# Kernel optimization log

Measured on AMD Instinct MI355X. Metric: run time of the kernel, lower is better.

Reference implementation:

```python
import jax, jax.numpy as jnp
import numpy as np
import math

L, D, H, FF, V, S = 6, 512, 8, 2048, 32000, 1024
DH = D // H
EPS = 1e-5

def _ln(x, w, b):
    mu = jnp.mean(x, -1, keepdims=True)
    var = jnp.mean(jnp.square(x - mu), -1, keepdims=True)
    return (x - mu) * jax.lax.rsqrt(var + EPS) * w + b

def setup_inputs() -> dict:
    key = jax.random.key(0)
    ks = jax.random.split(key, 32)
    s = 0.02
    inp = {
        'x': jax.random.randint(ks[0], (4, S), 0, V, dtype=jnp.int32),
        'mask': jnp.ones((4, S), dtype=jnp.int32),
        'emb': jax.random.normal(ks[1], (V, D), jnp.float32) * s,
        'pos': jax.random.normal(ks[2], (S, D), jnp.float32) * s,
        'Wq': jax.random.normal(ks[3], (L, D, D), jnp.float32) * s,
        'bq': jnp.zeros((L, D), jnp.float32),
        'Wk': jax.random.normal(ks[4], (L, D, D), jnp.float32) * s,
        'bk': jnp.zeros((L, D), jnp.float32),
        'Wv': jax.random.normal(ks[5], (L, D, D), jnp.float32) * s,
        'bv': jnp.zeros((L, D), jnp.float32),
        'Wo': jax.random.normal(ks[6], (L, D, D), jnp.float32) * s,
        'bo': jnp.zeros((L, D), jnp.float32),
        'rel_bias': jax.random.normal(ks[7], (L, 2 * S - 1, H), jnp.float32) * s,
        'scale': jnp.full((L,), math.sqrt(DH), jnp.float32),
        'n1w': jnp.ones((L, D), jnp.float32), 'n1b': jnp.zeros((L, D), jnp.float32),
        'n2w': jnp.ones((L, D), jnp.float32), 'n2b': jnp.zeros((L, D), jnp.float32),
        'f1w': jax.random.normal(ks[8], (L, D, FF), jnp.float32) * s,
        'f1b': jnp.zeros((L, FF), jnp.float32),
        'f2w': jax.random.normal(ks[9], (L, FF, D), jnp.float32) * s,
        'f2b': jnp.zeros((L, D), jnp.float32),
        'fnw': jnp.ones((D,), jnp.float32), 'fnb': jnp.zeros((D,), jnp.float32),
        'fcw': jax.random.normal(ks[10], (D, V), jnp.float32) * s,
        'fcb': jnp.zeros((V,), jnp.float32),
    }
    return inp

def reference(x, mask, emb, pos, Wq, bq, Wk, bk, Wv, bv, Wo, bo, rel_bias, scale,
              n1w, n1b, n2w, n2b, f1w, f1b, f2w, f2b, fnw, fnb, fcw, fcb):
    B, seq = x.shape
    h = emb[x] * jnp.float32(math.sqrt(D)) + pos[None, :seq, :]
    # relative position index table: j - i + seq - 1, values in [0, 2*seq-2]
    r = jnp.arange(seq)
    rp = r[None, :] - r[:, None] + seq - 1  # (S, S)
    # pairwise valid mask (b,1,S,S)
    m2 = (mask[:, None, None, :] * mask[:, None, :, None]) != 0
    for l in range(L):
        q = (h @ Wq[l] + bq[l]).reshape(B, seq, H, DH)
        k = (h @ Wk[l] + bk[l]).reshape(B, seq, H, DH)
        v = (h @ Wv[l] + bv[l]).reshape(B, seq, H, DH)
        scores = jnp.einsum('bihd,bjhd->bhij', q, k) / scale[l]
        bias = rel_bias[l][rp]                      # (S,S,H)
        scores = scores + jnp.transpose(bias, (2, 0, 1))[None]
        scores = jnp.where(m2, scores, -jnp.inf)    # masked_fill(mask==0, -inf)
        attn = jnp.einsum('bhij,bjhd->bihd', scores, v).reshape(B, seq, D)
        attn = attn @ Wo[l] + bo[l]
        h = _ln(h + attn, n1w[l], n1b[l])
        ff = jax.nn.gelu(h @ f1w[l] + f1b[l], approximate=False) @ f2w[l] + f2b[l]
        h = _ln(h + ff, n2w[l], n2b[l])
    h = _ln(h, fnw, fnb)
    return h @ fcw + fcb
```

## Files before the change

kernel.cpp:

```cpp
#include <hip/hip_runtime.h>
#include <cmath>

#define S_LEN  1024
#define DMODEL 512
#define NHEAD  8
#define DHEAD  64
#define FFDIM  2048
#define VOCAB  32000
#define NLAYER 6
#define BATCHN 4
#define ROWS   (BATCHN * S_LEN)

typedef float    f32x4 __attribute__((ext_vector_type(4)));
typedef _Float16 f16x4 __attribute__((ext_vector_type(4)));
typedef _Float16 f16x8 __attribute__((ext_vector_type(8)));

__device__ __forceinline__ void glds16(const _Float16* g, _Float16* l) {
    __builtin_amdgcn_global_load_lds(
        (const __attribute__((address_space(1))) void*)g,
        (__attribute__((address_space(3))) void*)l, 16, 0, 0);
}

template<int N> __device__ __forceinline__ void waitvm() {
    if constexpr (N == 0)      asm volatile("s_waitcnt vmcnt(0)" ::: "memory");
    else if constexpr (N == 3) asm volatile("s_waitcnt vmcnt(3)" ::: "memory");
    else if constexpr (N == 4) asm volatile("s_waitcnt vmcnt(4)" ::: "memory");
    else if constexpr (N == 6) asm volatile("s_waitcnt vmcnt(6)" ::: "memory");
}

template<int WM, int WN, int MT, int NT, int EPI, int OUT16, int SWZ8>
__global__ __launch_bounds__(WM * WN * 64)
void pgemm_k(const _Float16* __restrict__ A, long lda,
             const _Float16* __restrict__ Bt, long ldb,
             void* __restrict__ Cg, long ldc, int K,
             const float* __restrict__ bias)
{
    constexpr int T   = WM * WN * 64;
    constexpr int BMt = WM * MT * 16;
    constexpr int BNt = WN * NT * 16;
    constexpr int SR  = T / 4;
    constexpr int RA  = BMt / SR;
    constexpr int RB  = BNt / SR;
    constexpr int L   = RA + RB;
    constexpr int ASZ = BMt * 32, BSZ = BNt * 32;

    __shared__ _Float16 As[3 * ASZ];
    __shared__ _Float16 Bs[3 * BSZ];

    int bx = blockIdx.x, by = blockIdx.y;
    if (SWZ8) {
        int nb  = gridDim.x * gridDim.y;
        int id  = by * gridDim.x + bx;
        int id2 = (id & 7) * (nb >> 3) + (id >> 3);
        bx = id2 % gridDim.x;
        by = id2 / gridDim.x;
    }
    const int m0 = bx * BMt, n0 = by * BNt;

    const int t = threadIdx.x, w = t >> 6, lane = t & 63;
    const int sub = t >> 2, ch = t & 3;
    const int wm = w / WN, wn = w % WN;
    const int wrow = wm * MT * 16, wcol = wn * NT * 16;
    const int lr = lane & 15, hk = lane >> 4;

    f32x4 acc[MT][NT];
#pragma unroll
    for (int i = 0; i < MT; i++)
#pragma unroll
        for (int j = 0; j < NT; j++) acc[i][j] = f32x4{0.f, 0.f, 0.f, 0.f};

    const int nst = K >> 5;

    auto stage = [&](int tt) {
        const int kt = tt << 5;
        _Float16* Ad = &As[(tt % 3) * ASZ];
        _Float16* Bd = &Bs[(tt % 3) * BSZ];
#pragma unroll
        for (int i = 0; i < RA; i++) {
            int lrow = i * SR + sub;
            glds16(A + (long)(m0 + lrow) * lda + kt + ((ch ^ ((lrow >> 1) & 3)) << 3),
                   Ad + (i * SR + w * 16) * 32);
        }
#pragma unroll
        for (int i = 0; i < RB; i++) {
            int lrow = i * SR + sub;
            glds16(Bt + (long)(n0 + lrow) * ldb + kt + ((ch ^ ((lrow >> 1) & 3)) << 3),
                   Bd + (i * SR + w * 16) * 32);
        }
    };

    stage(0);
    stage(1);

    for (int tt = 0; tt < nst; ++tt) {
        if (tt < nst - 1) waitvm<L>(); else waitvm<0>();
        asm volatile("s_barrier" ::: "memory");
        if (tt + 2 < nst) stage(tt + 2);

        const _Float16* Ar = &As[(tt % 3) * ASZ];
        const _Float16* Br = &Bs[(tt % 3) * BSZ];
        f16x8 af[MT], bf[NT];
#pragma unroll
        for (int mi = 0; mi < MT; mi++) {
            int r = wrow + mi * 16 + lr;
            af[mi] = *(const f16x8*)&Ar[r * 32 + ((hk ^ ((r >> 1) & 3)) << 3)];
        }
#pragma unroll
        for (int ni = 0; ni < NT; ni++) {
            int r = wcol + ni * 16 + lr;
            bf[ni] = *(const f16x8*)&Br[r * 32 + ((hk ^ ((r >> 1) & 3)) << 3)];
        }
#pragma unroll
        for (int mi = 0; mi < MT; mi++)
#pragma unroll
            for (int ni = 0; ni < NT; ni++)
                acc[mi][ni] = __builtin_amdgcn_mfma_f32_16x16x32_f16(af[mi], bf[ni], acc[mi][ni], 0, 0, 0);
    }

    const int crow = hk * 4, ccol = lr;
#pragma unroll
    for (int mi = 0; mi < MT; mi++)
#pragma unroll
        for (int ni = 0; ni < NT; ni++)
#pragma unroll
            for (int q = 0; q < 4; q++) {
                int gm = m0 + wrow + mi * 16 + crow + q;
                int gn = n0 + wcol + ni * 16 + ccol;
                float v = acc[mi][ni][q];
                if (bias) v += bias[gn];
                if (EPI == 2) v = 0.5f * v * (1.0f + erff(v * 0.70710678118654752f));
                long ci = (long)gm * ldc + gn;
                if (OUT16) ((_Float16*)Cg)[ci] = (_Float16)v;
                else       ((float*)Cg)[ci] = v;
            }
}

__global__ __launch_bounds__(256)
void ktv_k(const _Float16* __restrict__ kt, const _Float16* __restrict__ vt,
           _Float16* __restrict__ M, const float* __restrict__ scale_p)
{
    const int z = blockIdx.x;
    const int wave = threadIdx.x >> 6, lane = threadIdx.x & 63;
    const int lr = lane & 15, lk = (lane >> 4) * 8;
    const long base = (long)z * DHEAD * S_LEN;

    f32x4 acc[4];
#pragma unroll
    for (int i = 0; i < 4; i++) acc[i] = f32x4{0.f, 0.f, 0.f, 0.f};

    for (int j = 0; j < S_LEN; j += 32) {
        f16x8 a = *(const f16x8*)&vt[base + (long)(wave * 16 + lr) * S_LEN + j + lk];
#pragma unroll
        for (int ni = 0; ni < 4; ni++) {
            f16x8 b = *(const f16x8*)&kt[base + (long)(ni * 16 + lr) * S_LEN + j + lk];
            acc[ni] = __builtin_amdgcn_mfma_f32_16x16x32_f16(a, b, acc[ni], 0, 0, 0);
        }
    }

    const float inv = 1.0f / scale_p[0];
    const int crow = (lane >> 4) * 4, ccol = lane & 15;
#pragma unroll
    for (int ni = 0; ni < 4; ni++)
#pragma unroll
        for (int q = 0; q < 4; q++) {
            int gm = wave * 16 + crow + q;
            int gn = ni * 16 + ccol;
            M[(long)z * 4096 + (long)gm * 64 + gn] = (_Float16)(acc[ni][q] * inv);
        }
}

__global__ __launch_bounds__(256)
void toep_k(const _Float16* __restrict__ dv,
            const _Float16* __restrict__ vt,
            const _Float16* __restrict__ q,
            const _Float16* __restrict__ M,
            _Float16* __restrict__ ao)
{
    __shared__ _Float16 Qs[64 * 64];
    __shared__ _Float16 Ms[64 * 64];
    __shared__ _Float16 Vs[2][64 * 64];
    __shared__ _Float16 dseg[1088];

    const int t = threadIdx.x, w = t >> 6, lane = t & 63;
    const int z = blockIdx.z, zb = z >> 3, zh = z & 7;
    const int m0 = blockIdx.x * 64;
    const int lr = lane & 15, hk = lane >> 4;
    const int rsw = lr & 7;
    const int swz = ((lane & 7) ^ (lane >> 3)) * 8;
    const int wrow = w * 16;

    const _Float16* qa = q  + (long)(zb * S_LEN + m0 + w * 16 + (lane >> 3)) * 1536 + zh * 64 + swz;
    const _Float16* ma = M  + (long)z * 4096 + (long)(w * 16 + (lane >> 3)) * 64 + swz;
    const _Float16* va = vt + (long)z * (DHEAD * S_LEN) + (long)(w * 16 + (lane >> 3)) * S_LEN + swz;

#pragma unroll
    for (int i = 0; i < 2; i++) glds16(qa + (long)i * 8 * 1536, &Qs[(w * 16 + i * 8) * 64]);
#pragma unroll
    for (int i = 0; i < 2; i++) glds16(ma + i * 8 * 64, &Ms[(w * 16 + i * 8) * 64]);
#pragma unroll
    for (int i = 0; i < 2; i++) glds16(va + (long)i * 8 * S_LEN, &Vs[0][(w * 16 + i * 8) * 64]);
    {
        const _Float16* dp = dv + zh * 2048 + (960 - m0);
        for (int i = t; i < 1088; i += 256) dseg[i] = dp[i];
    }
    __syncthreads();

    f32x4 acc[4];
#pragma unroll
    for (int i = 0; i < 4; i++) acc[i] = f32x4{0.f, 0.f, 0.f, 0.f};

#pragma unroll
    for (int kc = 0; kc < 64; kc += 32) {
        const int coff = ((((kc >> 3) + hk) ^ rsw) << 3);
        f16x8 aq = *(const f16x8*)&Qs[(wrow + lr) * 64 + coff];
#pragma unroll
        for (int ni = 0; ni < 4; ni++) {
            f16x8 bm = *(const f16x8*)&Ms[(ni * 16 + lr) * 64 + coff];
            acc[ni] = __builtin_amdgcn_mfma_f32_16x16x32_f16(aq, bm, acc[ni], 0, 0, 0);
        }
    }

    int cur = 0;
    for (int kt = 0; kt < S_LEN; kt += 64) {
        if (kt + 64 < S_LEN) {
#pragma unroll
            for (int i = 0; i < 2; i++)
                glds16(va + (long)i * 8 * S_LEN + kt + 64, &Vs[cur ^ 1][(w * 16 + i * 8) * 64]);
        }
#pragma unroll
        for (int kc = 0; kc < 64; kc += 32) {
            const int coff = ((((kc >> 3) + hk) ^ rsw) << 3);
            f16x8 at_;
            const int xb = kt + kc + hk * 8 + 63 - wrow - lr;
#pragma unroll
            for (int u = 0; u < 8; u++) at_[u] = dseg[xb + u];
#pragma unroll
            for (int ni = 0; ni < 4; ni++) {
                f16x8 bv_ = *(const f16x8*)&Vs[cur][(ni * 16 + lr) * 64 + coff];
                acc[ni] = __builtin_amdgcn_mfma_f32_16x16x32_f16(at_, bv_, acc[ni], 0, 0, 0);
            }
        }
        __syncthreads();
        cur ^= 1;
    }

    const int crow = (lane >> 4) * 4, ccol = lane & 15;
    const long cbase = (long)zb * (S_LEN * DMODEL) + zh * DHEAD;
#pragma unroll
    for (int ni = 0; ni < 4; ni++)
#pragma unroll
        for (int qq = 0; qq < 4; qq++) {
            int gm = m0 + wrow + crow + qq;
            int gn = ni * 16 + ccol;
            ao[cbase + (long)gm * DMODEL + gn] = (_Float16)acc[ni][qq];
        }
}

__global__ void embed_k(const int* __restrict__ x, const float* __restrict__ emb,
                        const float* __restrict__ pos, float* __restrict__ h,
                        _Float16* __restrict__ h16)
{
    int row = blockIdx.x;
    int s   = row & (S_LEN - 1);
    int tok = x[row];
    int c   = threadIdx.x * 4;
    f32x4 e = *(const f32x4*)(emb + (long)tok * DMODEL + c);
    f32x4 p = *(const f32x4*)(pos + (long)s * DMODEL + c);
    f32x4 o = e * 22.62741699796952f + p;
    *(f32x4*)(h + (long)row * DMODEL + c) = o;
    f16x4 o16;
#pragma unroll
    for (int j = 0; j < 4; j++) o16[j] = (_Float16)o[j];
    *(f16x4*)(h16 + (long)row * DMODEL + c) = o16;
}

__global__ void ln_k(const float* __restrict__ x, const float* __restrict__ add,
                     const float* __restrict__ w, const float* __restrict__ bb,
                     float* __restrict__ out, _Float16* __restrict__ out16)
{
    int row  = blockIdx.x;
    int lane = threadIdx.x;
    const float* xp = x + (long)row * DMODEL + lane * 8;
    f32x4 a = *(const f32x4*)xp;
    f32x4 b4 = *(const f32x4*)(xp + 4);
    if (add) {
        const float* ap = add + (long)row * DMODEL + lane * 8;
        a  += *(const f32x4*)ap;
        b4 += *(const f32x4*)(ap + 4);
    }
    float v[8] = {a[0],a[1],a[2],a[3],b4[0],b4[1],b4[2],b4[3]};
    float s = 0.f;
#pragma unroll
    for (int i = 0; i < 8; i++) s += v[i];
#pragma unroll
    for (int off = 32; off; off >>= 1) s += __shfl_xor(s, off);
    float mu = s * (1.0f / 512.0f);
    float d2 = 0.f;
#pragma unroll
    for (int i = 0; i < 8; i++) { v[i] -= mu; d2 += v[i] * v[i]; }
#pragma unroll
    for (int off = 32; off; off >>= 1) d2 += __shfl_xor(d2, off);
    float r = rsqrtf(d2 * (1.0f / 512.0f) + 1e-5f);
    const float* wp = w  + lane * 8;
    const float* bp = bb + lane * 8;
    float o[8];
#pragma unroll
    for (int i = 0; i < 8; i++) o[i] = v[i] * r * wp[i] + bp[i];
    float* op = out + (long)row * DMODEL + lane * 8;
    *(f32x4*)op       = f32x4{o[0], o[1], o[2], o[3]};
    *(f32x4*)(op + 4) = f32x4{o[4], o[5], o[6], o[7]};
    f16x8 o16;
#pragma unroll
    for (int i = 0; i < 8; i++) o16[i] = (_Float16)o[i];
    *(f16x8*)(out16 + (long)row * DMODEL + lane * 8) = o16;
}

__global__ void wcvt_k(const float* __restrict__ in, _Float16* __restrict__ out,
                       int R, int C, long inZ, long outZ)
{
    __shared__ float tile[32][33];
    int z = blockIdx.z;
    int c0 = blockIdx.x * 32, r0 = blockIdx.y * 32;
    int tx = threadIdx.x, ty = threadIdx.y;
#pragma unroll
    for (int i = 0; i < 4; i++)
        tile[ty + i * 8][tx] = in[(long)z * inZ + (long)(r0 + ty + i * 8) * C + c0 + tx];
    __syncthreads();
#pragma unroll
    for (int i = 0; i < 4; i++)
        out[(long)z * outZ + (long)(c0 + ty + i * 8) * R + r0 + tx] = (_Float16)tile[tx][ty + i * 8];
}

__global__ void tv16_k(const _Float16* __restrict__ qkv,
                       _Float16* __restrict__ kt, _Float16* __restrict__ vt)
{
    __shared__ _Float16 tile[32][33];
    int z = blockIdx.z;
    const _Float16* v = qkv + ((z < 32) ? 512 : 1024);
    _Float16* dst = (z < 32) ? kt : vt;
    int zz = z & 31;
    int b = zz >> 3, hh = zz & 7;
    int j0 = blockIdx.x * 32, d0 = blockIdx.y * 32;
    long ibase = (long)b * S_LEN * 1536 + hh * DHEAD;
    long obase = (long)zz * (DHEAD * S_LEN);
    int tx = threadIdx.x, ty = threadIdx.y;
#pragma unroll
    for (int i = 0; i < 4; i++)
        tile[ty + i * 8][tx] = v[ibase + (long)(j0 + ty + i * 8) * 1536 + d0 + tx];
    __syncthreads();
#pragma unroll
    for (int i = 0; i < 4; i++)
        dst[obase + (long)(d0 + ty + i * 8) * S_LEN + j0 + tx] = tile[tx][ty + i * 8];
}

__global__ void bcat_k(const float* __restrict__ bq, const float* __restrict__ bk,
                       const float* __restrict__ bv, float* __restrict__ o)
{
    int l = blockIdx.x, t = threadIdx.x;
    o[l * 1536 + t]        = bq[l * 512 + t];
    o[l * 1536 + 512 + t]  = bk[l * 512 + t];
    o[l * 1536 + 1024 + t] = bv[l * 512 + t];
}

__global__ void dvec_k(const float* __restrict__ rel, _Float16* __restrict__ dv)
{
    int lh = blockIdx.x;
    int l = lh >> 3, hh = lh & 7;
    for (int t = threadIdx.x; t < 2048; t += 256)
        dv[(long)lh * 2048 + t] = (t < 2047) ? (_Float16)rel[(long)l * 2047 * 8 + (long)t * 8 + hh]
                                             : (_Float16)0.0f;
}

extern "C" void kernel_launch(void* const* d_in, const int* in_sizes, int n_in,
                              void* d_out, int out_size, void* d_ws, size_t ws_size,
                              hipStream_t stream)
{
    (void)in_sizes; (void)n_in; (void)out_size; (void)ws_size;

    const int*   x    = (const int*)d_in[0];
    const float* emb  = (const float*)d_in[2];
    const float* pos  = (const float*)d_in[3];
    const float* Wq   = (const float*)d_in[4];
    const float* bq   = (const float*)d_in[5];
    const float* Wk   = (const float*)d_in[6];
    const float* bk   = (const float*)d_in[7];
    const float* Wv   = (const float*)d_in[8];
    const float* bv   = (const float*)d_in[9];
    const float* Wo   = (const float*)d_in[10];
    const float* bo   = (const float*)d_in[11];
    const float* rel  = (const float*)d_in[12];
    const float* scal = (const float*)d_in[13];
    const float* n1w  = (const float*)d_in[14];
    const float* n1b  = (const float*)d_in[15];
    const float* n2w  = (const float*)d_in[16];
    const float* n2b  = (const float*)d_in[17];
    const float* f1w  = (const float*)d_in[18];
    const float* f1b  = (const float*)d_in[19];
    const float* f2w  = (const float*)d_in[20];
    const float* f2b  = (const float*)d_in[21];
    const float* fnw  = (const float*)d_in[22];
    const float* fnb  = (const float*)d_in[23];
    const float* fcw  = (const float*)d_in[24];
    const float* fcb  = (const float*)d_in[25];

    char* ws = (char*)d_ws;
    size_t off = 0;
    auto alloc = [&](size_t bytes) { char* p = ws + off; off += (bytes + 255) & ~(size_t)255; return p; };
    float*    h      = (float*)alloc((size_t)ROWS * DMODEL * 4);
    float*    proj   = (float*)alloc((size_t)ROWS * DMODEL * 4);
    float*    ff2    = (float*)alloc((size_t)ROWS * DMODEL * 4);
    _Float16* h16    = (_Float16*)alloc((size_t)ROWS * DMODEL * 2);
    _Float16* qkv16  = (_Float16*)alloc((size_t)ROWS * 3 * DMODEL * 2);
    _Float16* kt16   = (_Float16*)alloc((size_t)ROWS * DMODEL * 2);
    _Float16* vt16   = (_Float16*)alloc((size_t)ROWS * DMODEL * 2);
    _Float16* ao16   = (_Float16*)alloc((size_t)ROWS * DMODEL * 2);
    _Float16* ff116  = (_Float16*)alloc((size_t)ROWS * FFDIM * 2);
    _Float16* M16    = (_Float16*)alloc((size_t)32 * 4096 * 2);
    _Float16* wqkvT  = (_Float16*)alloc((size_t)NLAYER * 3 * DMODEL * DMODEL * 2);
    _Float16* woT    = (_Float16*)alloc((size_t)NLAYER * DMODEL * DMODEL * 2);
    _Float16* f1T    = (_Float16*)alloc((size_t)NLAYER * DMODEL * FFDIM * 2);
    _Float16* f2T    = (_Float16*)alloc((size_t)NLAYER * DMODEL * FFDIM * 2);
    _Float16* fcT    = (_Float16*)alloc((size_t)VOCAB * DMODEL * 2);
    float*    bqkv   = (float*)alloc((size_t)NLAYER * 3 * DMODEL * 4);
    _Float16* dv16   = (_Float16*)alloc((size_t)NLAYER * NHEAD * 2048 * 2);

    dim3 bT(32, 8);

    wcvt_k<<<dim3(16, 16, NLAYER), bT, 0, stream>>>(Wq, wqkvT,               DMODEL, DMODEL, (long)DMODEL*DMODEL, (long)3*DMODEL*DMODEL);
    wcvt_k<<<dim3(16, 16, NLAYER), bT, 0, stream>>>(Wk, wqkvT + 512*512,     DMODEL, DMODEL, (long)DMODEL*DMODEL, (long)3*DMODEL*DMODEL);
    wcvt_k<<<dim3(16, 16, NLAYER), bT, 0, stream>>>(Wv, wqkvT + 2*512*512,   DMODEL, DMODEL, (long)DMODEL*DMODEL, (long)3*DMODEL*DMODEL);
    wcvt_k<<<dim3(16, 16, NLAYER), bT, 0, stream>>>(Wo, woT,                 DMODEL, DMODEL, (long)DMODEL*DMODEL, (long)DMODEL*DMODEL);
    wcvt_k<<<dim3(FFDIM/32, 16, NLAYER), bT, 0, stream>>>(f1w, f1T,          DMODEL, FFDIM,  (long)DMODEL*FFDIM,  (long)DMODEL*FFDIM);
    wcvt_k<<<dim3(16, FFDIM/32, NLAYER), bT, 0, stream>>>(f2w, f2T,          FFDIM,  DMODEL, (long)DMODEL*FFDIM,  (long)DMODEL*FFDIM);
    wcvt_k<<<dim3(VOCAB/32, 16, 1), bT, 0, stream>>>(fcw, fcT,               DMODEL, VOCAB,  0, 0);
    bcat_k<<<NLAYER, 512, 0, stream>>>(bq, bk, bv, bqkv);
    dvec_k<<<NLAYER * NHEAD, 256, 0, stream>>>(rel, dv16);

    embed_k<<<ROWS, 128, 0, stream>>>(x, emb, pos, h, h16);

    for (int l = 0; l < NLAYER; l++) {
        const long lw  = (long)l * DMODEL * DMODEL;
        const long lff = (long)l * DMODEL * FFDIM;

        pgemm_k<1,4,4,2,0,1,0><<<dim3(64, 12), 256, 0, stream>>>(
            h16, DMODEL, wqkvT + l * 3 * 512 * 512, DMODEL,
            qkv16, 3 * DMODEL, DMODEL, bqkv + l * 3 * DMODEL);

        tv16_k<<<dim3(32, 2, 64), bT, 0, stream>>>(qkv16, kt16, vt16);

        ktv_k<<<32, 256, 0, stream>>>(kt16, vt16, M16, scal + l);

        toep_k<<<dim3(16, 1, 32), 256, 0, stream>>>(
            dv16 + (long)l * NHEAD * 2048, vt16, qkv16, M16, ao16);

        pgemm_k<1,4,4,2,0,0,0><<<dim3(64, 4), 256, 0, stream>>>(
            ao16, DMODEL, woT + lw, DMODEL, proj, DMODEL, DMODEL, bo + l * DMODEL);

        ln_k<<<ROWS, 64, 0, stream>>>(h, proj, n1w + l * DMODEL, n1b + l * DMODEL, h, h16);

        pgemm_k<1,4,4,2,2,1,0><<<dim3(64, 16), 256, 0, stream>>>(
            h16, DMODEL, f1T + lff, DMODEL, ff116, FFDIM, DMODEL, f1b + l * FFDIM);

        pgemm_k<1,4,4,2,0,0,0><<<dim3(64, 4), 256, 0, stream>>>(
            ff116, FFDIM, f2T + lff, FFDIM, ff2, DMODEL, FFDIM, f2b + l * DMODEL);

        ln_k<<<ROWS, 64, 0, stream>>>(h, ff2, n2w + l * DMODEL, n2b + l * DMODEL, h, h16);
    }

    ln_k<<<ROWS, 64, 0, stream>>>(h, nullptr, fnw, fnb, proj, h16);

    pgemm_k<2,2,4,4,0,0,1><<<dim3(32, VOCAB / 128), 256, 0, stream>>>(
        h16, DMODEL, fcT, DMODEL, (float*)d_out, VOCAB, DMODEL, fcb);
}
```

Measured before the change: 1.368 ms.

## Triple-buffer V tiles in toep_k, enable tile swizzle and nontemporal logits stores

```diff
diff --git a/kernel.cpp b/kernel.cpp
--- a/kernel.cpp
+++ b/kernel.cpp
@@ -23,12 +23,13 @@
 
 template<int N> __device__ __forceinline__ void waitvm() {
     if constexpr (N == 0)      asm volatile("s_waitcnt vmcnt(0)" ::: "memory");
+    else if constexpr (N == 2) asm volatile("s_waitcnt vmcnt(2)" ::: "memory");
     else if constexpr (N == 3) asm volatile("s_waitcnt vmcnt(3)" ::: "memory");
     else if constexpr (N == 4) asm volatile("s_waitcnt vmcnt(4)" ::: "memory");
     else if constexpr (N == 6) asm volatile("s_waitcnt vmcnt(6)" ::: "memory");
 }
 
-template<int WM, int WN, int MT, int NT, int EPI, int OUT16, int SWZ8>
+template<int WM, int WN, int MT, int NT, int EPI, int OUT16, int SWZ8, int NTS>
 __global__ __launch_bounds__(WM * WN * 64)
 void pgemm_k(const _Float16* __restrict__ A, long lda,
              const _Float16* __restrict__ Bt, long ldb,
@@ -130,8 +131,14 @@
                 if (bias) v += bias[gn];
                 if (EPI == 2) v = 0.5f * v * (1.0f + erff(v * 0.70710678118654752f));
                 long ci = (long)gm * ldc + gn;
-                if (OUT16) ((_Float16*)Cg)[ci] = (_Float16)v;
-                else       ((float*)Cg)[ci] = v;
+                if (OUT16) {
+                    _Float16 hv = (_Float16)v;
+                    if (NTS) __builtin_nontemporal_store(hv, &((_Float16*)Cg)[ci]);
+                    else     ((_Float16*)Cg)[ci] = hv;
+                } else {
+                    if (NTS) __builtin_nontemporal_store(v, &((float*)Cg)[ci]);
+                    else     ((float*)Cg)[ci] = v;
+                }
             }
 }
 
@@ -178,7 +185,7 @@
 {
     __shared__ _Float16 Qs[64 * 64];
     __shared__ _Float16 Ms[64 * 64];
-    __shared__ _Float16 Vs[2][64 * 64];
+    __shared__ _Float16 Vs[3][64 * 64];
     __shared__ _Float16 dseg[1088];
 
     const int t = threadIdx.x, w = t >> 6, lane = t & 63;
@@ -193,17 +200,27 @@
     const _Float16* ma = M  + (long)z * 4096 + (long)(w * 16 + (lane >> 3)) * 64 + swz;
     const _Float16* va = vt + (long)z * (DHEAD * S_LEN) + (long)(w * 16 + (lane >> 3)) * S_LEN + swz;
 
-#pragma unroll
-    for (int i = 0; i < 2; i++) glds16(qa + (long)i * 8 * 1536, &Qs[(w * 16 + i * 8) * 64]);
-#pragma unroll
-    for (int i = 0; i < 2; i++) glds16(ma + i * 8 * 64, &Ms[(w * 16 + i * 8) * 64]);
-#pragma unroll
-    for (int i = 0; i < 2; i++) glds16(va + (long)i * 8 * S_LEN, &Vs[0][(w * 16 + i * 8) * 64]);
     {
         const _Float16* dp = dv + zh * 2048 + (960 - m0);
         for (int i = t; i < 1088; i += 256) dseg[i] = dp[i];
     }
-    __syncthreads();
+    waitvm<0>();
+
+    auto stageV = [&](int tt) {
+#pragma unroll
+        for (int i = 0; i < 2; i++)
+            glds16(va + (long)i * 8 * S_LEN + (tt << 6), &Vs[tt % 3][(w * 16 + i * 8) * 64]);
+    };
+
+#pragma unroll
+    for (int i = 0; i < 2; i++) glds16(qa + (long)i * 8 * 1536, &Qs[(w * 16 + i * 8) * 64]);
+#pragma unroll
+    for (int i = 0; i < 2; i++) glds16(ma + i * 8 * 64, &Ms[(w * 16 + i * 8) * 64]);
+    stageV(0);
+    stageV(1);
+
+    asm volatile("s_waitcnt vmcnt(4) lgkmcnt(0)" ::: "memory");
+    asm volatile("s_barrier" ::: "memory");
 
     f32x4 acc[4];
 #pragma unroll
@@ -220,13 +237,13 @@
         }
     }
 
-    int cur = 0;
-    for (int kt = 0; kt < S_LEN; kt += 64) {
-        if (kt + 64 < S_LEN) {
-#pragma unroll
-            for (int i = 0; i < 2; i++)
-                glds16(va + (long)i * 8 * S_LEN + kt + 64, &Vs[cur ^ 1][(w * 16 + i * 8) * 64]);
-        }
+    for (int tt = 0; tt < 16; ++tt) {
+        if (tt < 15) waitvm<2>(); else waitvm<0>();
+        asm volatile("s_barrier" ::: "memory");
+        if (tt + 2 < 16) stageV(tt + 2);
+
+        const int kt = tt << 6;
+        const _Float16* Vr = Vs[tt % 3];
 #pragma unroll
         for (int kc = 0; kc < 64; kc += 32) {
             const int coff = ((((kc >> 3) + hk) ^ rsw) << 3);
@@ -236,12 +253,10 @@
             for (int u = 0; u < 8; u++) at_[u] = dseg[xb + u];
 #pragma unroll
             for (int ni = 0; ni < 4; ni++) {
-                f16x8 bv_ = *(const f16x8*)&Vs[cur][(ni * 16 + lr) * 64 + coff];
+                f16x8 bv_ = *(const f16x8*)&Vr[(ni * 16 + lr) * 64 + coff];
                 acc[ni] = __builtin_amdgcn_mfma_f32_16x16x32_f16(at_, bv_, acc[ni], 0, 0, 0);
             }
         }
-        __syncthreads();
-        cur ^= 1;
     }
 
     const int crow = (lane >> 4) * 4, ccol = lane & 15;
@@ -442,7 +457,7 @@
         const long lw  = (long)l * DMODEL * DMODEL;
         const long lff = (long)l * DMODEL * FFDIM;
 
-        pgemm_k<1,4,4,2,0,1,0><<<dim3(64, 12), 256, 0, stream>>>(
+        pgemm_k<1,4,4,2,0,1,1,0><<<dim3(64, 12), 256, 0, stream>>>(
             h16, DMODEL, wqkvT + l * 3 * 512 * 512, DMODEL,
             qkv16, 3 * DMODEL, DMODEL, bqkv + l * 3 * DMODEL);
 
@@ -453,15 +468,15 @@
         toep_k<<<dim3(16, 1, 32), 256, 0, stream>>>(
             dv16 + (long)l * NHEAD * 2048, vt16, qkv16, M16, ao16);
 
-        pgemm_k<1,4,4,2,0,0,0><<<dim3(64, 4), 256, 0, stream>>>(
+        pgemm_k<1,4,4,2,0,0,1,0><<<dim3(64, 4), 256, 0, stream>>>(
             ao16, DMODEL, woT + lw, DMODEL, proj, DMODEL, DMODEL, bo + l * DMODEL);
 
         ln_k<<<ROWS, 64, 0, stream>>>(h, proj, n1w + l * DMODEL, n1b + l * DMODEL, h, h16);
 
-        pgemm_k<1,4,4,2,2,1,0><<<dim3(64, 16), 256, 0, stream>>>(
+        pgemm_k<1,4,4,2,2,1,1,0><<<dim3(64, 16), 256, 0, stream>>>(
             h16, DMODEL, f1T + lff, DMODEL, ff116, FFDIM, DMODEL, f1b + l * FFDIM);
 
-        pgemm_k<1,4,4,2,0,0,0><<<dim3(64, 4), 256, 0, stream>>>(
+        pgemm_k<1,4,4,2,0,0,1,0><<<dim3(64, 4), 256, 0, stream>>>(
             ff116, FFDIM, f2T + lff, FFDIM, ff2, DMODEL, FFDIM, f2b + l * DMODEL);
 
         ln_k<<<ROWS, 64, 0, stream>>>(h, ff2, n2w + l * DMODEL, n2b + l * DMODEL, h, h16);
@@ -469,6 +484,6 @@
 
     ln_k<<<ROWS, 64, 0, stream>>>(h, nullptr, fnw, fnb, proj, h16);
 
-    pgemm_k<2,2,4,4,0,0,1><<<dim3(32, VOCAB / 128), 256, 0, stream>>>(
+    pgemm_k<2,2,4,4,0,0,1,1><<<dim3(32, VOCAB / 128), 256, 0, stream>>>(
         h16, DMODEL, fcT, DMODEL, (float*)d_out, VOCAB, DMODEL, fcb);
 }
```

Measured after the change: 1.234 ms. -9.8%, faster.
